# Kernel optimization log

Hardware: AMD Instinct MI355X
Metric: run time of the kernel (lower is better)

The kernel has to match this reference:

```python
import jax, jax.numpy as jnp
import numpy as np

K = 7          # neighborhood kernel size (7x7)
NH = 8         # num heads


def _nbr_idx(n):
    # NATTEN-style clamped windows: window start = clip(i - K//2, 0, n-K)
    pos = jnp.arange(n)
    start = jnp.clip(pos - K // 2, 0, n - K)          # (n,)
    idx = start[:, None] + jnp.arange(K)[None, :]     # (n, K) absolute key positions
    rel = idx - pos[:, None] + (K - 1)                # (n, K) in [0, 2K-2] for rpb lookup
    return idx, rel


def _forward(x, w_qkv, b_qkv, rpb, w_proj, b_proj, w_fc1, b_fc1, w_fc2, b_fc2):
    B, C, H, W = x.shape
    hd = C // NH
    scale = hd ** -0.5

    # ---- neighborhood attention (norm0 = Identity) ----
    xp = jnp.transpose(x, (0, 2, 3, 1))                           # (B,H,W,C)
    qkv = xp @ w_qkv + b_qkv                                      # (B,H,W,3C)
    qkv = qkv.reshape(B, H, W, 3, NH, hd)
    q = qkv[:, :, :, 0] * scale                                   # (B,H,W,nh,hd)
    k = qkv[:, :, :, 1]
    v = qkv[:, :, :, 2]

    idx_h, rel_h = _nbr_idx(H)                                    # (H,K)
    idx_w, rel_w = _nbr_idx(W)                                    # (W,K)

    # gather 7x7 neighborhoods: (B,H,K,W,K,nh,hd)
    k_nbr = k[:, idx_h][:, :, :, idx_w]
    v_nbr = v[:, idx_h][:, :, :, idx_w]

    # attention logits: (B,H,W,nh,K,K)
    attn = jnp.einsum('bxynd,bxiyjnd->bxynij', q, k_nbr)
    # relative positional bias: rpb (nh, 2K-1, 2K-1) -> (nh,H,K,W,K)
    bias = rpb[:, rel_h][:, :, :, rel_w]                          # (nh,H,K,W,K)
    attn = attn + jnp.transpose(bias, (1, 3, 0, 2, 4))[None]      # (B,H,W,nh,K,K)

    attn = jax.nn.softmax(attn.reshape(B, H, W, NH, K * K), axis=-1)
    attn = attn.reshape(B, H, W, NH, K, K)

    out = jnp.einsum('bxynij,bxiyjnd->bxynd', attn, v_nbr)        # (B,H,W,nh,hd)
    out = out.reshape(B, H, W, C) @ w_proj + b_proj               # (B,H,W,C)
    x1 = jnp.transpose(out, (0, 3, 1, 2)) + x                     # residual skip0

    # ---- MLP (1x1-conv style, channels-first; norm1 = Identity) ----
    h = jnp.einsum('bchw,cf->bfhw', x1, w_fc1) + b_fc1[None, :, None, None]
    h = jax.nn.gelu(h, approximate=False)                         # torch nn.GELU (erf)
    y = jnp.einsum('bfhw,fc->bchw', h, w_fc2) + b_fc2[None, :, None, None]
    return y + x1                                                 # residual skip1


def setup_inputs() -> dict:
    key = jax.random.key(0)
    B, C, H, W = 1, 256, 64, 128
    hid = int(C * 2.0)
    ks = jax.random.split(key, 8)
    s = 0.02
    return {
        'x': jax.random.normal(ks[0], (B, C, H, W), jnp.float32),
        'w_qkv': jax.random.normal(ks[1], (C, 3 * C), jnp.float32) * s,
        'b_qkv': jnp.zeros((3 * C,), jnp.float32),
        'rpb': jax.random.normal(ks[2], (NH, 2 * K - 1, 2 * K - 1), jnp.float32) * s,
        'w_proj': jax.random.normal(ks[3], (C, C), jnp.float32) * s,
        'b_proj': jnp.zeros((C,), jnp.float32),
        'w_fc1': jax.random.normal(ks[4], (C, hid), jnp.float32) * s,
        'b_fc1': jnp.zeros((hid,), jnp.float32),
        'w_fc2': jax.random.normal(ks[5], (hid, C), jnp.float32) * s,
        'b_fc2': jnp.zeros((C,), jnp.float32),
    }


def reference(x, w_qkv, b_qkv, rpb, w_proj, b_proj, w_fc1, b_fc1, w_fc2, b_fc2):
    return _forward(x, w_qkv, b_qkv, rpb, w_proj, b_proj, w_fc1, b_fc1, w_fc2, b_fc2)
```

## Files before the change

kernel.cpp:

```cpp
#include <hip/hip_runtime.h>

typedef unsigned short ushort;
typedef short bf16x8 __attribute__((ext_vector_type(8)));
typedef float f32x4 __attribute__((ext_vector_type(4)));

static __device__ __forceinline__ ushort f2b(float f) {
  unsigned u = __builtin_bit_cast(unsigned, f);
  u = (u + 0x7fffu + ((u >> 16) & 1u)) >> 16;
  return (ushort)u;
}
static __device__ __forceinline__ float b2f(ushort b) {
  return __builtin_bit_cast(float, (unsigned)b << 16);
}

static __device__ __forceinline__ void gll16(const ushort* g, ushort* l) {
  __builtin_amdgcn_global_load_lds(
      (const __attribute__((address_space(1))) void*)g,
      (__attribute__((address_space(3))) void*)l, 16, 0, 0);
}

__global__ __launch_bounds__(256) void prep_kernel(
    const float* __restrict__ x,
    const float* __restrict__ w_qkv, const float* __restrict__ w_proj,
    const float* __restrict__ w_fc1, const float* __restrict__ w_fc2,
    ushort* __restrict__ xb, ushort* __restrict__ wqkvT,
    ushort* __restrict__ wprojT, ushort* __restrict__ wfc1T,
    ushort* __restrict__ wfc2T)
{
  __shared__ float tile[32][33];
  int t = blockIdx.x;
  const float* src; ushort* dst; int R, Nc, r0, c0;
  if (t < 2048)              { src = x;      dst = xb;     R = 256; Nc = 8192; r0 = (t >> 8) * 32; c0 = (t & 255) * 32; }
  else if ((t -= 2048) < 192){ src = w_qkv;  dst = wqkvT;  R = 256; Nc = 768;  r0 = (t / 24) * 32; c0 = (t % 24) * 32; }
  else if ((t -= 192) < 64)  { src = w_proj; dst = wprojT; R = 256; Nc = 256;  r0 = (t / 8) * 32;  c0 = (t % 8) * 32; }
  else if ((t -= 64) < 128)  { src = w_fc1;  dst = wfc1T;  R = 256; Nc = 512;  r0 = (t / 16) * 32; c0 = (t % 16) * 32; }
  else           { t -= 128;   src = w_fc2;  dst = wfc2T;  R = 512; Nc = 256;  r0 = (t / 8) * 32;  c0 = (t % 8) * 32; }

  const int tx = threadIdx.x & 31, ty = threadIdx.x >> 5;
  #pragma unroll
  for (int i = 0; i < 4; i++)
    tile[ty + i * 8][tx] = src[(size_t)(r0 + ty + i * 8) * Nc + c0 + tx];
  __syncthreads();
  #pragma unroll
  for (int i = 0; i < 4; i++)
    dst[(size_t)(c0 + ty + i * 8) * R + r0 + tx] = f2b(tile[tx][ty + i * 8]);
}

template<int EPI, int KD>
__global__ __launch_bounds__(256) void gemm_mfma(
    const ushort* __restrict__ A, const ushort* __restrict__ Bt,
    const float* __restrict__ bias, const float* __restrict__ R,
    const ushort* __restrict__ RS,
    void* __restrict__ C0, void* __restrict__ C1,
    int M, int N)
{
  __shared__ __attribute__((aligned(16))) ushort As[64 * 128];
  __shared__ __attribute__((aligned(16))) ushort Bs[64 * 128];

  const int bm = blockIdx.y * 64;
  const int bn = blockIdx.x * 64;
  const int t  = threadIdx.x;
  const int w    = t >> 6;
  const int lane = t & 63;
  const int wm = (w & 1) * 32;
  const int wn = (w >> 1) * 32;
  const int lm = lane & 15;
  const int kq = lane >> 4;

  const int rl  = lane >> 4;
  const int cbx = (lane & 15) << 4;
  const int xr  = (lm & 7) << 4;

  f32x4 acc[2][2] = {};

  #pragma unroll
  for (int k0 = 0; k0 < KD; k0 += 128) {
    #pragma unroll
    for (int s = 0; s < 4; s++) {
      const int c = w * 4 + s;
      const int r = c * 4 + rl;
      const int off = (cbx ^ ((r & 7) << 4)) >> 1;
      gll16(A  + (size_t)(bm + r) * KD + k0 + off, As + c * 512);
      gll16(Bt + (size_t)(bn + r) * KD + k0 + off, Bs + c * 512);
    }
    __syncthreads();

    #pragma unroll
    for (int ks = 0; ks < 4; ks++) {
      const int kb = ks * 64 + (kq << 4);
      const int cs = kb ^ xr;
      bf16x8 a0 = *(const bf16x8*)((const char*)As + (wm + lm)      * 256 + cs);
      bf16x8 a1 = *(const bf16x8*)((const char*)As + (wm + 16 + lm) * 256 + cs);
      bf16x8 b0 = *(const bf16x8*)((const char*)Bs + (wn + lm)      * 256 + cs);
      bf16x8 b1 = *(const bf16x8*)((const char*)Bs + (wn + 16 + lm) * 256 + cs);
      acc[0][0] = __builtin_amdgcn_mfma_f32_16x16x32_bf16(a0, b0, acc[0][0], 0, 0, 0);
      acc[0][1] = __builtin_amdgcn_mfma_f32_16x16x32_bf16(a0, b1, acc[0][1], 0, 0, 0);
      acc[1][0] = __builtin_amdgcn_mfma_f32_16x16x32_bf16(a1, b0, acc[1][0], 0, 0, 0);
      acc[1][1] = __builtin_amdgcn_mfma_f32_16x16x32_bf16(a1, b1, acc[1][1], 0, 0, 0);
    }
    __syncthreads();
  }

  #pragma unroll
  for (int ti = 0; ti < 2; ti++) {
    #pragma unroll
    for (int tj = 0; tj < 2; tj++) {
      const int n  = bn + wn + tj * 16 + lm;
      const int m0 = bm + wm + ti * 16 + kq * 4;
      if (EPI == 0) {
        if (n < 512) {
          #pragma unroll
          for (int r = 0; r < 4; r++)
            ((ushort*)C0)[(size_t)(m0 + r) * N + n] = f2b(acc[ti][tj][r] + bias[n]);
        } else {
          ushort4 st;
          st.x = f2b(acc[ti][tj][0] + bias[n]);
          st.y = f2b(acc[ti][tj][1] + bias[n]);
          st.z = f2b(acc[ti][tj][2] + bias[n]);
          st.w = f2b(acc[ti][tj][3] + bias[n]);
          *(ushort4*)((ushort*)C1 + (size_t)(n - 512) * 8192 + m0) = st;
        }
      }
    }
  }
}

__global__ __launch_bounds__(256, 4) void natt_mfma(
    const ushort* __restrict__ qkv, const ushort* __restrict__ vT,
    const float* __restrict__ rpb, ushort* __restrict__ att)
{
  __shared__ __attribute__((aligned(16))) ushort Plds[4][7][16][40];
  __shared__ float Rlds[4][176];

  const int w    = threadIdx.x >> 6;
  const int lane = threadIdx.x & 63;
  const int l  = lane & 15;
  const int q  = lane >> 4;
  const int tile = blockIdx.x;
  const int n    = blockIdx.y * 4 + w;
  const int ph  = tile >> 3;
  const int pw0 = (tile & 7) << 4;
  const int p0  = ph * 128 + pw0;

  int sh = ph - 3;  sh = sh < 0 ? 0 : (sh > 57 ? 57 : sh);
  int sb = pw0 - 3; sb = sb < 0 ? 0 : sb;
  const int sba = sb & ~7;

  const float L2E = 1.44269504f;
  for (int idx = lane; idx < 169; idx += 64)
    Rlds[w][idx] = rpb[n * 169 + idx] * L2E;

  bf16x8 qf = *(const bf16x8*)(qkv + (size_t)(p0 + l) * 768 + n * 32 + q * 8);

  const float KSC = 0.17677669529663689f * 1.44269504f;
  const int relh0 = sh - ph + 6;
  float rsum[4] = {0.f, 0.f, 0.f, 0.f};

  #pragma unroll
  for (int h = 0; h < 2; h++) {
    f32x4 s[7] = {};
    #pragma unroll
    for (int i = 0; i < 7; i++) {
      const int rowp = (sh + i) * 128;
      int jc = sba + h * 16 + l;
      jc = jc > 127 ? 127 : jc;
      bf16x8 kf = *(const bf16x8*)(qkv + (size_t)(rowp + jc) * 768 + 256 + n * 32 + q * 8);
      s[i] = __builtin_amdgcn_mfma_f32_16x16x32_bf16(qf, kf, s[i], 0, 0, 0);
    }
    #pragma unroll
    for (int r = 0; r < 4; r++) {
      const int pw = pw0 + q * 4 + r;
      int sw = pw - 3; sw = sw < 0 ? 0 : (sw > 121 ? 121 : sw);
      const int jc = sba + h * 16 + l;
      const bool valid = (unsigned)(jc - sw) <= 6u;
      int relw = jc - pw + 6;
      relw = relw < 0 ? 0 : (relw > 12 ? 12 : relw);
      #pragma unroll
      for (int i = 0; i < 7; i++) {
        float b = Rlds[w][(relh0 + i) * 13 + relw];
        float v = s[i][r] * KSC + b;
        v = valid ? v : -1e30f;
        float e = exp2f(v);
        rsum[r] += e;
        Plds[w][i][q * 4 + r][h * 16 + l] = f2b(e);
      }
    }
  }

  #pragma unroll
  for (int r = 0; r < 4; r++) {
    rsum[r] += __shfl_xor(rsum[r], 1);
    rsum[r] += __shfl_xor(rsum[r], 2);
    rsum[r] += __shfl_xor(rsum[r], 4);
    rsum[r] += __shfl_xor(rsum[r], 8);
  }

  f32x4 o[2] = {};
  #pragma unroll
  for (int i = 0; i < 7; i++) {
    bf16x8 pf = *(const bf16x8*)(&Plds[w][i][l][q * 8]);
    const int rowp = (sh + i) * 128;
    #pragma unroll
    for (int dh = 0; dh < 2; dh++) {
      bf16x8 vf = *(const bf16x8*)(vT + (size_t)(n * 32 + dh * 16 + l) * 8192
                                      + rowp + sba + q * 8);
      o[dh] = __builtin_amdgcn_mfma_f32_16x16x32_bf16(pf, vf, o[dh], 0, 0, 0);
    }
  }

  #pragma unroll
  for (int r = 0; r < 4; r++) {
    const float inv = 1.0f / rsum[r];
    #pragma unroll
    for (int dh = 0; dh < 2; dh++)
      att[(size_t)(p0 + q * 4 + r) * 256 + n * 32 + dh * 16 + l] = f2b(o[dh][r] * inv);
  }
}

__global__ __launch_bounds__(512, 4) void mlp_fused(
    const ushort* __restrict__ att, const ushort* __restrict__ wprojT,
    const ushort* __restrict__ wfc1T, const ushort* __restrict__ wfc2T,
    const float* __restrict__ b_proj, const float* __restrict__ b_fc1,
    const float* __restrict__ b_fc2, const float* __restrict__ xres,
    float* __restrict__ out)
{
  __shared__ __attribute__((aligned(16))) ushort X1[16 * 256];
  __shared__ __attribute__((aligned(16))) ushort Hs[16 * 256];

  const int bm   = blockIdx.x * 16;
  const int w    = threadIdx.x >> 6;
  const int lane = threadIdx.x & 63;
  const int lm   = lane & 15;
  const int kq   = lane >> 4;
  const int wn   = w * 32;

  {
    f32x4 accp[2] = {};
    #pragma unroll
    for (int kk = 0; kk < 8; kk++) {
      const int ko = kk * 32 + kq * 8;
      bf16x8 a = *(const bf16x8*)(att + (size_t)(bm + lm) * 256 + ko);
      #pragma unroll
      for (int tj = 0; tj < 2; tj++) {
        const int n = wn + tj * 16 + lm;
        bf16x8 b = *(const bf16x8*)(wprojT + (size_t)n * 256 + ko);
        accp[tj] = __builtin_amdgcn_mfma_f32_16x16x32_bf16(a, b, accp[tj], 0, 0, 0);
      }
    }
    #pragma unroll
    for (int tj = 0; tj < 2; tj++) {
      const int n = wn + tj * 16 + lm;
      const float bp = b_proj[n];
      float4 xr = *(const float4*)(xres + (size_t)n * 8192 + bm + kq * 4);
      const float* xp = &xr.x;
      #pragma unroll
      for (int r = 0; r < 4; r++) {
        const int m = kq * 4 + r;
        X1[m * 256 + (n ^ ((m & 7) << 3))] = f2b(accp[tj][r] + bp + xp[r]);
      }
    }
  }
  __syncthreads();

  f32x4 acco[2] = {};
  #pragma unroll
  for (int hf = 0; hf < 2; hf++) {
    f32x4 acch[2] = {};
    #pragma unroll
    for (int kk = 0; kk < 8; kk++) {
      const int ko = kk * 32 + kq * 8;
      bf16x8 a = *(const bf16x8*)(&X1[lm * 256 + (ko ^ ((lm & 7) << 3))]);
      #pragma unroll
      for (int tj = 0; tj < 2; tj++) {
        const int n = wn + tj * 16 + lm;
        bf16x8 b = *(const bf16x8*)(wfc1T + (size_t)(hf * 256 + n) * 256 + ko);
        acch[tj] = __builtin_amdgcn_mfma_f32_16x16x32_bf16(a, b, acch[tj], 0, 0, 0);
      }
    }
    #pragma unroll
    for (int tj = 0; tj < 2; tj++) {
      const int n = wn + tj * 16 + lm;
      const float b1 = b_fc1[hf * 256 + n];
      #pragma unroll
      for (int r = 0; r < 4; r++) {
        const int m = kq * 4 + r;
        float v = acch[tj][r] + b1;
        v = 0.5f * v * (1.0f + erff(v * 0.70710678118f));
        Hs[m * 256 + (n ^ ((m & 7) << 3))] = f2b(v);
      }
    }
    __syncthreads();

    #pragma unroll
    for (int kk = 0; kk < 8; kk++) {
      const int ko = kk * 32 + kq * 8;
      bf16x8 a = *(const bf16x8*)(&Hs[lm * 256 + (ko ^ ((lm & 7) << 3))]);
      #pragma unroll
      for (int tj = 0; tj < 2; tj++) {
        const int n = wn + tj * 16 + lm;
        bf16x8 b = *(const bf16x8*)(wfc2T + (size_t)n * 512 + hf * 256 + ko);
        acco[tj] = __builtin_amdgcn_mfma_f32_16x16x32_bf16(a, b, acco[tj], 0, 0, 0);
      }
    }
    __syncthreads();
  }

  #pragma unroll
  for (int tj = 0; tj < 2; tj++) {
    const int n  = wn + tj * 16 + lm;
    const int m0 = kq * 4;
    const float b2 = b_fc2[n];
    float4 v;
    float* vp = &v.x;
    #pragma unroll
    for (int r = 0; r < 4; r++) {
      const int m = m0 + r;
      vp[r] = acco[tj][r] + b2 + b2f(X1[m * 256 + (n ^ ((m & 7) << 3))]);
    }
    *(float4*)(out + (size_t)n * 8192 + bm + m0) = v;
  }
}

extern "C" void kernel_launch(void* const* d_in, const int* in_sizes, int n_in,
                              void* d_out, int out_size, void* d_ws, size_t ws_size,
                              hipStream_t stream)
{
  const float* x      = (const float*)d_in[0];
  const float* w_qkv  = (const float*)d_in[1];
  const float* b_qkv  = (const float*)d_in[2];
  const float* rpb    = (const float*)d_in[3];
  const float* w_proj = (const float*)d_in[4];
  const float* b_proj = (const float*)d_in[5];
  const float* w_fc1  = (const float*)d_in[6];
  const float* b_fc1  = (const float*)d_in[7];
  const float* w_fc2  = (const float*)d_in[8];
  const float* b_fc2  = (const float*)d_in[9];
  float* out = (float*)d_out;

  const int M = 8192;
  char* ws = (char*)d_ws;
  ushort* xb     = (ushort*)(ws);
  ushort* qkv    = (ushort*)(ws + 4194304);
  ushort* wqkvT  = (ushort*)(ws + 20971520);
  ushort* wprojT = (ushort*)(ws + 21364736);
  ushort* wfc1T  = (ushort*)(ws + 21495808);
  ushort* wfc2T  = (ushort*)(ws + 21757952);
  ushort* vT     = (ushort*)(ws + 22020096);
  ushort* att = xb;

  dim3 blk(256);

  prep_kernel<<<dim3(2560), blk, 0, stream>>>(
      x, w_qkv, w_proj, w_fc1, w_fc2, xb, wqkvT, wprojT, wfc1T, wfc2T);

  gemm_mfma<0, 256><<<dim3(768 / 64, M / 64), blk, 0, stream>>>(
      xb, wqkvT, b_qkv, nullptr, nullptr, qkv, vT, M, 768);

  natt_mfma<<<dim3(512, 2), blk, 0, stream>>>(qkv, vT, rpb, att);

  mlp_fused<<<dim3(512), dim3(512), 0, stream>>>(
      att, wprojT, wfc1T, wfc2T, b_proj, b_fc1, b_fc2, x, out);
}
```

Measured before the change: 151.2 us.

## Stage MLP weight tiles through double-buffered LDS with async global-to-LDS loads

```diff
diff --git a/kernel.cpp b/kernel.cpp
--- a/kernel.cpp
+++ b/kernel.cpp
@@ -217,13 +217,14 @@
   }
 }
 
-__global__ __launch_bounds__(512, 4) void mlp_fused(
+__global__ __launch_bounds__(256, 3) void mlp_fused(
     const ushort* __restrict__ att, const ushort* __restrict__ wprojT,
     const ushort* __restrict__ wfc1T, const ushort* __restrict__ wfc2T,
     const float* __restrict__ b_proj, const float* __restrict__ b_fc1,
     const float* __restrict__ b_fc2, const float* __restrict__ xres,
     float* __restrict__ out)
 {
+  __shared__ __attribute__((aligned(16))) ushort Bs[2][64 * 128];
   __shared__ __attribute__((aligned(16))) ushort X1[16 * 256];
   __shared__ __attribute__((aligned(16))) ushort Hs[16 * 256];
 
@@ -232,92 +233,126 @@
   const int lane = threadIdx.x & 63;
   const int lm   = lane & 15;
   const int kq   = lane >> 4;
-  const int wn   = w * 32;
-
-  {
-    f32x4 accp[2] = {};
-    #pragma unroll
-    for (int kk = 0; kk < 8; kk++) {
-      const int ko = kk * 32 + kq * 8;
-      bf16x8 a = *(const bf16x8*)(att + (size_t)(bm + lm) * 256 + ko);
-      #pragma unroll
-      for (int tj = 0; tj < 2; tj++) {
-        const int n = wn + tj * 16 + lm;
-        bf16x8 b = *(const bf16x8*)(wprojT + (size_t)n * 256 + ko);
-        accp[tj] = __builtin_amdgcn_mfma_f32_16x16x32_bf16(a, b, accp[tj], 0, 0, 0);
-      }
-    }
-    #pragma unroll
-    for (int tj = 0; tj < 2; tj++) {
-      const int n = wn + tj * 16 + lm;
-      const float bp = b_proj[n];
-      float4 xr = *(const float4*)(xres + (size_t)n * 8192 + bm + kq * 4);
-      const float* xp = &xr.x;
-      #pragma unroll
-      for (int r = 0; r < 4; r++) {
-        const int m = kq * 4 + r;
-        X1[m * 256 + (n ^ ((m & 7) << 3))] = f2b(accp[tj][r] + bp + xp[r]);
-      }
-    }
-  }
-  __syncthreads();
-
-  f32x4 acco[2] = {};
-  #pragma unroll
-  for (int hf = 0; hf < 2; hf++) {
-    f32x4 acch[2] = {};
-    #pragma unroll
-    for (int kk = 0; kk < 8; kk++) {
-      const int ko = kk * 32 + kq * 8;
-      bf16x8 a = *(const bf16x8*)(&X1[lm * 256 + (ko ^ ((lm & 7) << 3))]);
-      #pragma unroll
-      for (int tj = 0; tj < 2; tj++) {
-        const int n = wn + tj * 16 + lm;
-        bf16x8 b = *(const bf16x8*)(wfc1T + (size_t)(hf * 256 + n) * 256 + ko);
-        acch[tj] = __builtin_amdgcn_mfma_f32_16x16x32_bf16(a, b, acch[tj], 0, 0, 0);
-      }
-    }
-    #pragma unroll
-    for (int tj = 0; tj < 2; tj++) {
-      const int n = wn + tj * 16 + lm;
-      const float b1 = b_fc1[hf * 256 + n];
-      #pragma unroll
-      for (int r = 0; r < 4; r++) {
-        const int m = kq * 4 + r;
-        float v = acch[tj][r] + b1;
-        v = 0.5f * v * (1.0f + erff(v * 0.70710678118f));
-        Hs[m * 256 + (n ^ ((m & 7) << 3))] = f2b(v);
-      }
-    }
+  const int wnn  = w * 16;
+  const int rl   = lane >> 4;
+  const int swl  = (lane & 15) << 3;
+
+  bf16x8 af[2][4];
+  #pragma unroll
+  for (int kt = 0; kt < 2; kt++)
+    #pragma unroll
+    for (int ks = 0; ks < 4; ks++)
+      af[kt][ks] = *(const bf16x8*)(att + (size_t)(bm + lm) * 256
+                                    + kt * 128 + ks * 32 + kq * 8);
+  float4 xr4[4];
+  float bpv[4], bf1v[2][4], bf2v[4];
+  #pragma unroll
+  for (int np = 0; np < 4; np++) {
+    const int n = np * 64 + wnn + lm;
+    xr4[np]     = *(const float4*)(xres + (size_t)n * 8192 + bm + kq * 4);
+    bpv[np]     = b_proj[n];
+    bf1v[0][np] = b_fc1[n];
+    bf1v[1][np] = b_fc1[256 + n];
+    bf2v[np]    = b_fc2[n];
+  }
+
+  auto stage = [&](int b, const ushort* __restrict__ src, int ldk, int row0, int col0) {
+    #pragma unroll
+    for (int s = 0; s < 4; s++) {
+      const int c = w * 4 + s;
+      const int n = c * 4 + rl;
+      gll16(src + (size_t)(row0 + n) * ldk + col0 + (swl ^ ((n & 7) << 3)),
+            &Bs[b][c * 512]);
+    }
+  };
+  auto compP = [&](int b, int kt, f32x4& a4) {
+    #pragma unroll
+    for (int ks = 0; ks < 4; ks++) {
+      const int kc = ks * 32 + kq * 8;
+      const int nr = wnn + lm;
+      bf16x8 bfr = *(const bf16x8*)(&Bs[b][nr * 128 + (kc ^ ((nr & 7) << 3))]);
+      a4 = __builtin_amdgcn_mfma_f32_16x16x32_bf16(af[kt][ks], bfr, a4, 0, 0, 0);
+    }
+  };
+  auto compS = [&](int b, const ushort* __restrict__ S, int kt, f32x4& a4) {
+    #pragma unroll
+    for (int ks = 0; ks < 4; ks++) {
+      const int kc = ks * 32 + kq * 8;
+      const int ac = kt * 128 + kc;
+      bf16x8 a = *(const bf16x8*)(S + lm * 256 + (ac ^ ((lm & 7) << 3)));
+      const int nr = wnn + lm;
+      bf16x8 bfr = *(const bf16x8*)(&Bs[b][nr * 128 + (kc ^ ((nr & 7) << 3))]);
+      a4 = __builtin_amdgcn_mfma_f32_16x16x32_bf16(a, bfr, a4, 0, 0, 0);
+    }
+  };
+  auto projEpi = [&](int np, f32x4& a4) {
+    const int n = np * 64 + wnn + lm;
+    const float* xp = (const float*)&xr4[np];
+    #pragma unroll
+    for (int r = 0; r < 4; r++) {
+      const int m = kq * 4 + r;
+      X1[m * 256 + (n ^ ((m & 7) << 3))] = f2b(a4[r] + bpv[np] + xp[r]);
+    }
+  };
+  auto fc1Epi = [&](int hf, int np, f32x4& a4) {
+    const int n = np * 64 + wnn + lm;
+    #pragma unroll
+    for (int r = 0; r < 4; r++) {
+      const int m = kq * 4 + r;
+      float v = a4[r] + bf1v[hf][np];
+      v = 0.5f * v * (1.0f + erff(v * 0.70710678118f));
+      Hs[m * 256 + (n ^ ((m & 7) << 3))] = f2b(v);
+    }
+  };
+
+  constexpr int WHICH[40] = {0,0,0,0,0,0,0,0, 1,1,1,1,1,1,1,1, 2,2,2,2,2,2,2,2,
+                             1,1,1,1,1,1,1,1, 2,2,2,2,2,2,2,2};
+  constexpr int ROW0[40]  = {0,0,64,64,128,128,192,192, 0,0,64,64,128,128,192,192,
+                             0,0,64,64,128,128,192,192, 256,256,320,320,384,384,448,448,
+                             0,0,64,64,128,128,192,192};
+  constexpr int COL0[40]  = {0,128,0,128,0,128,0,128, 0,128,0,128,0,128,0,128,
+                             0,128,0,128,0,128,0,128, 0,128,0,128,0,128,0,128,
+                             256,384,256,384,256,384,256,384};
+  const ushort* const srcs[3] = {wprojT, wfc1T, wfc2T};
+  const int ldks[3] = {256, 256, 512};
+
+  f32x4 accp = {}, acch = {};
+  f32x4 acco[4] = {};
+
+  stage(0, srcs[WHICH[0]], ldks[WHICH[0]], ROW0[0], COL0[0]);
+
+  #pragma unroll
+  for (int p = 0; p < 40; p++) {
+    const int buf = p & 1;
     __syncthreads();
-
-    #pragma unroll
-    for (int kk = 0; kk < 8; kk++) {
-      const int ko = kk * 32 + kq * 8;
-      bf16x8 a = *(const bf16x8*)(&Hs[lm * 256 + (ko ^ ((lm & 7) << 3))]);
-      #pragma unroll
-      for (int tj = 0; tj < 2; tj++) {
-        const int n = wn + tj * 16 + lm;
-        bf16x8 b = *(const bf16x8*)(wfc2T + (size_t)n * 512 + hf * 256 + ko);
-        acco[tj] = __builtin_amdgcn_mfma_f32_16x16x32_bf16(a, b, acco[tj], 0, 0, 0);
-      }
-    }
-    __syncthreads();
-  }
-
-  #pragma unroll
-  for (int tj = 0; tj < 2; tj++) {
-    const int n  = wn + tj * 16 + lm;
-    const int m0 = kq * 4;
-    const float b2 = b_fc2[n];
+    if (p < 39)
+      stage(buf ^ 1, srcs[WHICH[p + 1]], ldks[WHICH[p + 1]], ROW0[p + 1], COL0[p + 1]);
+    const int np = (p >> 1) & 3;
+    const int kt = p & 1;
+    if (WHICH[p] == 0) {
+      if (kt == 0) accp = f32x4{};
+      compP(buf, kt, accp);
+      if (kt == 1) projEpi(np, accp);
+    } else if (WHICH[p] == 1) {
+      if (kt == 0) acch = f32x4{};
+      compS(buf, X1, kt, acch);
+      if (kt == 1) fc1Epi(p >= 24 ? 1 : 0, np, acch);
+    } else {
+      compS(buf, Hs, kt, acco[np]);
+    }
+  }
+
+  #pragma unroll
+  for (int np = 0; np < 4; np++) {
+    const int n = np * 64 + wnn + lm;
     float4 v;
     float* vp = &v.x;
     #pragma unroll
     for (int r = 0; r < 4; r++) {
-      const int m = m0 + r;
-      vp[r] = acco[tj][r] + b2 + b2f(X1[m * 256 + (n ^ ((m & 7) << 3))]);
-    }
-    *(float4*)(out + (size_t)n * 8192 + bm + m0) = v;
+      const int m = kq * 4 + r;
+      vp[r] = acco[np][r] + bf2v[np] + b2f(X1[m * 256 + (n ^ ((m & 7) << 3))]);
+    }
+    *(float4*)(out + (size_t)n * 8192 + bm + kq * 4) = v;
   }
 }
 
@@ -358,6 +393,6 @@
 
   natt_mfma<<<dim3(512, 2), blk, 0, stream>>>(qkv, vT, rpb, att);
 
-  mlp_fused<<<dim3(512), dim3(512), 0, stream>>>(
+  mlp_fused<<<dim3(512), dim3(256), 0, stream>>>(
       att, wprojT, wfc1T, wfc2T, b_proj, b_fc1, b_fc2, x, out);
 }
```

Measured after the change: 394.5 us. 161% more time.
